# Optimization experiments

Measured on AMD Instinct MI355X. Metric: run time of the kernel, lower is better.

Reference implementation:

```python
import jax, jax.numpy as jnp
import numpy as np

SCALE = 8      # scale_factor from map_to_mat_info
PATCH = 32     # up_delta - low_delta + 1 == right_delta - left_delta + 1 (uniform interior patches)


def setup_inputs() -> dict:
    key = jax.random.key(0)
    mat_h, mat_w = 160, 160
    H = (mat_h - 1) * SCALE + PATCH  # 1304: deltas (0,31,0,31) -> no border clipping
    W = (mat_w - 1) * SCALE + PATCH
    x = jax.random.normal(key, (1, 3, H, W), dtype=jnp.float32)
    rgb_weight = jnp.array([0.299, 0.587, 0.114], dtype=jnp.float32).reshape(1, 3, 1, 1)
    return {"x": x, "rgb_weight": rgb_weight, "mat_h": mat_h, "mat_w": mat_w}


def reference(x, rgb_weight, mat_h, mat_w):
    P = PATCH
    # RGB -> grayscale (convert_gray branch for in_channels == 3)
    gray = jnp.sum(x * rgb_weight, axis=1)[0]  # (H, W)
    # Gather all overlapping PxP patches at stride SCALE -> (mat_h, mat_w, P, P)
    rows = (jnp.arange(mat_h) * SCALE)[:, None] + jnp.arange(P)[None, :]  # (mat_h, P)
    cols = (jnp.arange(mat_w) * SCALE)[:, None] + jnp.arange(P)[None, :]  # (mat_w, P)
    p = gray[rows.reshape(-1)].reshape(mat_h, P, -1)              # (mat_h, P, W)
    p = p[:, :, cols.reshape(-1)].reshape(mat_h, P, mat_w, P)     # (mat_h, P, mat_w, P)
    patches = jnp.transpose(p, (0, 2, 1, 3))                      # (mat_h, mat_w, P, P)
    # torch.rfft(signal_ndim=2, onesided=False) == full 2D FFT; power = re^2 + im^2
    F = jnp.fft.fft2(patches)
    log_power = jnp.log(F.real * F.real + F.imag * F.imag + 1.0)
    # High-frequency region sums (h == w == P, static)
    lo = P // 2 - P // 4 - 1   # 7
    up = P // 2 + P // 4       # 24
    r1 = jnp.sum(log_power[..., lo:up + 1, :], axis=(-2, -1))
    r2 = jnp.sum(log_power[..., up + 1:, lo:up + 1], axis=(-2, -1))
    r3 = jnp.sum(log_power[..., :lo, lo:up + 1], axis=(-2, -1))
    mat = (r1 + r2 + r3)[None, None]  # (1, 1, mat_h, mat_w)
    return mat / jnp.max(mat)
```

## Files before the change

### kernel.cpp

```cpp
#include <hip/hip_runtime.h>
#include <math.h>

#define SCALE 8
#define PSZ 32

__device__ constexpr float C32[16] = {
     1.000000000000000f,  0.980785280403230f,  0.923879532511287f,  0.831469612302545f,
     0.707106781186548f,  0.555570233019602f,  0.382683432365090f,  0.195090322016128f,
     0.000000000000000f, -0.195090322016128f, -0.382683432365090f, -0.555570233019602f,
    -0.707106781186548f, -0.831469612302545f, -0.923879532511287f, -0.980785280403230f };
__device__ constexpr float S32[16] = {
     0.000000000000000f,  0.195090322016128f,  0.382683432365090f,  0.555570233019602f,
     0.707106781186548f,  0.831469612302545f,  0.923879532511287f,  0.980785280403230f,
     1.000000000000000f,  0.980785280403230f,  0.923879532511287f,  0.831469612302545f,
     0.707106781186548f,  0.555570233019602f,  0.382683432365090f,  0.195090322016128f };

__device__ __forceinline__ constexpr int brev5(int i) {
    return ((i & 1) << 4) | ((i & 2) << 2) | (i & 4) | ((i & 8) >> 2) | ((i & 16) >> 4);
}

__device__ __forceinline__ void fft32(float re[PSZ], float im[PSZ]) {
#pragma unroll
    for (int i = 0; i < 32; ++i) {
        const int j = brev5(i);
        if (j > i) {
            float t = re[i]; re[i] = re[j]; re[j] = t;
            t = im[i]; im[i] = im[j]; im[j] = t;
        }
    }
#pragma unroll
    for (int s = 1; s <= 5; ++s) {
        const int m = 1 << s;
        const int h = m >> 1;
        const int tstep = 32 >> s;
#pragma unroll
        for (int k = 0; k < 32; k += m) {
#pragma unroll
            for (int j = 0; j < h; ++j) {
                const float wr = C32[j * tstep];
                const float wi = -S32[j * tstep];
                const int a = k + j;
                const int b = k + j + h;
                const float tr = wr * re[b] - wi * im[b];
                const float ti = wr * im[b] + wi * re[b];
                re[b] = re[a] - tr; im[b] = im[a] - ti;
                re[a] = re[a] + tr; im[a] = im[a] + ti;
            }
        }
    }
}

__device__ __forceinline__ unsigned pack_bf2(float hi, float lo) {
    const unsigned uh = __float_as_uint(hi) + 0x8000u;
    const unsigned ul = __float_as_uint(lo) + 0x8000u;
    return (uh & 0xFFFF0000u) | (ul >> 16);
}
__device__ __forceinline__ float bf_hi(unsigned u) { return __uint_as_float(u & 0xFFFF0000u); }
__device__ __forceinline__ float bf_lo(unsigned u) { return __uint_as_float(u << 16); }

__global__ __launch_bounds__(256) void gray_kernel(
        const float* __restrict__ x, const float* __restrict__ w,
        float* __restrict__ g, int n4, long long HW) {
    const int i = blockIdx.x * 256 + threadIdx.x;
    if (i >= n4) return;
    const float w0 = w[0], w1 = w[1], w2 = w[2];
    const float4 a = reinterpret_cast<const float4*>(x)[i];
    const float4 b = reinterpret_cast<const float4*>(x + HW)[i];
    const float4 c = reinterpret_cast<const float4*>(x + 2 * HW)[i];
    float4 o;
    o.x = w0 * a.x + w1 * b.x + w2 * c.x;
    o.y = w0 * a.y + w1 * b.y + w2 * c.y;
    o.z = w0 * a.z + w1 * b.z + w2 * c.z;
    o.w = w0 * a.w + w1 * b.w + w2 * c.w;
    reinterpret_cast<float4*>(g)[i] = o;
}

template <bool GRAY_PRE>
__global__ __launch_bounds__(128) void hfdft_patch_kernel(
        const float* __restrict__ x, const float* __restrict__ w,
        float* __restrict__ out, int H, int W, int mat_h, int mat_w) {
    __shared__ unsigned cb[8 * 528];

    const int tid = threadIdx.x;
    const int wid = tid >> 6;
    const int lane = tid & 63;
    const int P0 = blockIdx.x * 8 + wid * 4;
    const int total = mat_h * mat_w;
    const long long HW = (long long)H * W;
    unsigned* cbw = cb + wid * 4 * 528;

    {
        const int g = lane >> 5, r = lane & 31;
        int pA = P0 + 2 * g;
        if (pA > total - 1) pA = total - 1;
        int pB = pA + 1; if (pB > total - 1) pB = total - 1;
        const int phA = pA / mat_w, pwA = pA % mat_w;
        const int phB = pB / mat_w, pwB = pB % mat_w;
        const bool adj = (phA == phB) && (pwB == pwA + 1);

        float re[PSZ], im[PSZ];
        if (GRAY_PRE) {
            if (adj) {
                const int base = (phA * SCALE + r) * W + pwA * SCALE;
                const float4* g4 = reinterpret_cast<const float4*>(x + base);
                float win[40];
#pragma unroll
                for (int q = 0; q < 10; ++q) {
                    const float4 v = g4[q];
                    win[4 * q + 0] = v.x; win[4 * q + 1] = v.y;
                    win[4 * q + 2] = v.z; win[4 * q + 3] = v.w;
                }
#pragma unroll
                for (int i = 0; i < PSZ; ++i) { re[i] = win[i]; im[i] = win[i + 8]; }
            } else {
                const int baseA = (phA * SCALE + r) * W + pwA * SCALE;
                const int baseB = (phB * SCALE + r) * W + pwB * SCALE;
#pragma unroll
                for (int i = 0; i < PSZ; ++i) { re[i] = x[baseA + i]; im[i] = x[baseB + i]; }
            }
        } else {
            const float w0 = w[0], w1 = w[1], w2 = w[2];
            if (adj && ((W & 3) == 0)) {
                const int base = (phA * SCALE + r) * W + pwA * SCALE;
                const float4* a4 = reinterpret_cast<const float4*>(x + base);
                const float4* b4 = reinterpret_cast<const float4*>(x + HW + base);
                const float4* c4 = reinterpret_cast<const float4*>(x + 2 * HW + base);
                float win[40];
#pragma unroll
                for (int q = 0; q < 10; ++q) {
                    const float4 a = a4[q], b = b4[q], c = c4[q];
                    win[4 * q + 0] = w0 * a.x + w1 * b.x + w2 * c.x;
                    win[4 * q + 1] = w0 * a.y + w1 * b.y + w2 * c.y;
                    win[4 * q + 2] = w0 * a.z + w1 * b.z + w2 * c.z;
                    win[4 * q + 3] = w0 * a.w + w1 * b.w + w2 * c.w;
                }
#pragma unroll
                for (int i = 0; i < PSZ; ++i) { re[i] = win[i]; im[i] = win[i + 8]; }
            } else {
                const int baseA = (phA * SCALE + r) * W + pwA * SCALE;
                const int baseB = (phB * SCALE + r) * W + pwB * SCALE;
#pragma unroll
                for (int i = 0; i < PSZ; ++i) {
                    re[i] = w0 * x[baseA + i] + w1 * x[HW + baseA + i] + w2 * x[2 * HW + baseA + i];
                    im[i] = w0 * x[baseB + i] + w1 * x[HW + baseB + i] + w2 * x[2 * HW + baseB + i];
                }
            }
        }

        fft32(re, im);

        unsigned* cbA = cbw + (2 * g) * 528;
        unsigned* cbB = cbA + 528;
        cbA[r] = pack_bf2(re[0], re[16]);
        cbB[r] = pack_bf2(im[0], im[16]);
#pragma unroll
        for (int k = 1; k <= 15; ++k) {
            const int m = 32 - k;
            const float far_ = 0.5f * (re[k] + re[m]);
            const float fai_ = 0.5f * (im[k] - im[m]);
            const float fbr_ = 0.5f * (im[k] + im[m]);
            const float fbi_ = 0.5f * (re[m] - re[k]);
            cbA[k * 33 + r] = pack_bf2(far_, fai_);
            cbB[k * 33 + r] = pack_bf2(fbr_, fbi_);
        }
    }

    asm volatile("s_waitcnt lgkmcnt(0)" ::: "memory");

    {
        const int pl = lane >> 4, slot = lane & 15;
        const int p = P0 + pl;
        const unsigned* cbp = cbw + pl * 528 + slot * 33;

        float cre[PSZ], cim[PSZ];
#pragma unroll
        for (int r2 = 0; r2 < PSZ; ++r2) {
            const unsigned u = cbp[r2];
            cre[r2] = bf_hi(u);
            cim[r2] = bf_lo(u);
        }

        fft32(cre, cim);

        float s0 = 0.0f, s1 = 0.0f;
        if (slot == 0) {
#pragma unroll
            for (int kr = 0; kr <= 16; ++kr) {
                const int m = (32 - kr) & 31;
                const float g0r = 0.5f * (cre[kr] + cre[m]);
                const float g0i = 0.5f * (cim[kr] - cim[m]);
                const float g1r = 0.5f * (cim[kr] + cim[m]);
                const float g1i = 0.5f * (cre[m] - cre[kr]);
                const float w0c = (kr >= 7 ? 1.0f : 0.0f) + ((kr >= 8 && kr <= 15) ? 1.0f : 0.0f);
                const float w16c = 1.0f + ((kr >= 1 && kr <= 15) ? 1.0f : 0.0f);
                if (w0c > 0.0f)
                    s0 = fmaf(w0c, __logf(g0r * g0r + g0i * g0i + 1.0f), s0);
                s1 = fmaf(w16c, __logf(g1r * g1r + g1i * g1i + 1.0f), s1);
            }
        } else {
            const float b1f = (slot >= 7) ? 1.0f : 0.0f;
            const float m1f = (slot >= 8) ? 1.0f : 0.0f;
#pragma unroll
            for (int kr = 0; kr < 32; ++kr) {
                const float lp = __logf(cre[kr] * cre[kr] + cim[kr] * cim[kr] + 1.0f);
                float wgt;
                if (kr >= 8 && kr <= 24)      wgt = 2.0f;
                else if (kr == 7)             wgt = 1.0f + m1f;
                else if (kr == 25)            wgt = b1f + 1.0f;
                else                          wgt = b1f + m1f;
                if (kr & 1) s1 = fmaf(wgt, lp, s1);
                else        s0 = fmaf(wgt, lp, s0);
            }
        }
        float s = s0 + s1;

#pragma unroll
        for (int off = 8; off >= 1; off >>= 1) s += __shfl_xor(s, off, 16);
        if (slot == 0 && p < total) out[p] = s;
    }
}

__global__ __launch_bounds__(1024) void max_kernel(
        const float* __restrict__ sums, int n, unsigned* __restrict__ mx) {
    __shared__ float sm[16];
    float m = 0.0f;
    for (int i = blockIdx.x * 1024 + threadIdx.x; i < n; i += gridDim.x * 1024)
        m = fmaxf(m, sums[i]);
#pragma unroll
    for (int off = 32; off >= 1; off >>= 1) m = fmaxf(m, __shfl_xor(m, off, 64));
    if ((threadIdx.x & 63) == 0) sm[threadIdx.x >> 6] = m;
    __syncthreads();
    if (threadIdx.x == 0) {
#pragma unroll
        for (int i = 1; i < 16; ++i) m = fmaxf(m, sm[i]);
        atomicMax(mx, __float_as_uint(m));
    }
}

__global__ __launch_bounds__(256) void norm_kernel(
        float* __restrict__ out, int n, const unsigned* __restrict__ mx) {
    const int i = blockIdx.x * 256 + threadIdx.x;
    if (i < n) out[i] = out[i] / __uint_as_float(mx[0]);
}

extern "C" void kernel_launch(void* const* d_in, const int* in_sizes, int n_in,
                              void* d_out, int out_size, void* d_ws, size_t ws_size,
                              hipStream_t stream) {
    const float* x = (const float*)d_in[0];
    const float* w = (const float*)d_in[1];
    float* out = (float*)d_out;

    const int HWi = in_sizes[0] / 3;
    const int H = (int)(sqrt((double)HWi) + 0.5);
    const int W = H;
    const long long HW = (long long)H * W;
    const int mat = (int)(sqrt((double)out_size) + 0.5);
    const int total = mat * mat;
    const int blocksA = (total + 7) / 8;

    unsigned* maxbuf = (unsigned*)d_ws;
    float* gray = (float*)((char*)d_ws + 256);
    const size_t need = 256 + (size_t)HW * 4;

    hipMemsetAsync(maxbuf, 0, 4, stream);

    if (ws_size >= need && (W & 3) == 0) {
        const int n4 = (int)(HW / 4);
        hipLaunchKernelGGL(gray_kernel, dim3((n4 + 255) / 256), dim3(256), 0, stream,
                           x, w, gray, n4, HW);
        hipLaunchKernelGGL((hfdft_patch_kernel<true>), dim3(blocksA), dim3(128), 0, stream,
                           gray, w, out, H, W, mat, mat);
    } else {
        hipLaunchKernelGGL((hfdft_patch_kernel<false>), dim3(blocksA), dim3(128), 0, stream,
                           x, w, out, H, W, mat, mat);
    }
    hipLaunchKernelGGL(max_kernel, dim3(8), dim3(1024), 0, stream, out, total, maxbuf);
    hipLaunchKernelGGL(norm_kernel, dim3((total + 255) / 256), dim3(256), 0, stream,
                       out, total, maxbuf);
}
```

Baseline: 47.57 us.

## Split patch FFT into shared row-FFT pass and per-patch column-FFT pass

```diff
diff --git a/kernel.cpp b/kernel.cpp
--- a/kernel.cpp
+++ b/kernel.cpp
@@ -75,6 +75,112 @@
     reinterpret_cast<float4*>(g)[i] = o;
 }
 
+__global__ __launch_bounds__(256, 4) void rowfft_kernel(
+        const float* __restrict__ g, unsigned* __restrict__ spec,
+        int H, int W, int mat_w) {
+    const int cpairs = mat_w >> 1;
+    const int t = blockIdx.x * 256 + threadIdx.x;
+    if (t >= H * cpairs) return;
+    const int y = t / cpairs, cp = t - y * cpairs;
+    const int c0 = 2 * cp;
+
+    const float4* g4 = reinterpret_cast<const float4*>(g + (size_t)y * W + (size_t)c0 * SCALE);
+    float win[40];
+#pragma unroll
+    for (int q = 0; q < 10; ++q) {
+        const float4 v = g4[q];
+        win[4 * q + 0] = v.x; win[4 * q + 1] = v.y;
+        win[4 * q + 2] = v.z; win[4 * q + 3] = v.w;
+    }
+    float re[PSZ], im[PSZ];
+#pragma unroll
+    for (int i = 0; i < PSZ; ++i) { re[i] = win[i]; im[i] = win[i + 8]; }
+
+    fft32(re, im);
+
+    unsigned outA[16], outB[16];
+    outA[0] = pack_bf2(re[0], re[16]);
+    outB[0] = pack_bf2(im[0], im[16]);
+#pragma unroll
+    for (int k = 1; k <= 15; ++k) {
+        const int m = 32 - k;
+        const float far_ = 0.5f * (re[k] + re[m]);
+        const float fai_ = 0.5f * (im[k] - im[m]);
+        const float fbr_ = 0.5f * (im[k] + im[m]);
+        const float fbi_ = 0.5f * (re[m] - re[k]);
+        outA[k] = pack_bf2(far_, fai_);
+        outB[k] = pack_bf2(fbr_, fbi_);
+    }
+    uint4* s4 = reinterpret_cast<uint4*>(spec + ((size_t)y * mat_w + c0) * 16);
+#pragma unroll
+    for (int q = 0; q < 4; ++q)
+        s4[q] = make_uint4(outA[4 * q], outA[4 * q + 1], outA[4 * q + 2], outA[4 * q + 3]);
+#pragma unroll
+    for (int q = 0; q < 4; ++q)
+        s4[4 + q] = make_uint4(outB[4 * q], outB[4 * q + 1], outB[4 * q + 2], outB[4 * q + 3]);
+}
+
+__global__ __launch_bounds__(128, 4) void colfft_kernel(
+        const unsigned* __restrict__ spec, float* __restrict__ out,
+        int mat_h, int mat_w) {
+    const int tid = threadIdx.x;
+    const int wid = tid >> 6, lane = tid & 63;
+    const int pl = lane >> 4, slot = lane & 15;
+    const int total = mat_h * mat_w;
+    int p = blockIdx.x * 8 + wid * 4 + pl;
+    if (p > total - 1) p = total - 1;
+    const int ph = p / mat_w, pw = p - ph * mat_w;
+
+    const unsigned* sp = spec + ((size_t)(ph * SCALE) * mat_w + pw) * 16 + slot;
+    const size_t rstride = (size_t)mat_w * 16;
+
+    float cre[PSZ], cim[PSZ];
+#pragma unroll
+    for (int r2 = 0; r2 < PSZ; ++r2) {
+        const unsigned u = sp[r2 * rstride];
+        cre[r2] = bf_hi(u);
+        cim[r2] = bf_lo(u);
+    }
+
+    fft32(cre, cim);
+
+    float s0 = 0.0f, s1 = 0.0f;
+    if (slot == 0) {
+#pragma unroll
+        for (int kr = 0; kr <= 16; ++kr) {
+            const int m = (32 - kr) & 31;
+            const float g0r = 0.5f * (cre[kr] + cre[m]);
+            const float g0i = 0.5f * (cim[kr] - cim[m]);
+            const float g1r = 0.5f * (cim[kr] + cim[m]);
+            const float g1i = 0.5f * (cre[m] - cre[kr]);
+            const float w0c = (kr >= 7 ? 1.0f : 0.0f) + ((kr >= 8 && kr <= 15) ? 1.0f : 0.0f);
+            const float w16c = 1.0f + ((kr >= 1 && kr <= 15) ? 1.0f : 0.0f);
+            if (w0c > 0.0f)
+                s0 = fmaf(w0c, __logf(g0r * g0r + g0i * g0i + 1.0f), s0);
+            s1 = fmaf(w16c, __logf(g1r * g1r + g1i * g1i + 1.0f), s1);
+        }
+    } else {
+        const float b1f = (slot >= 7) ? 1.0f : 0.0f;
+        const float m1f = (slot >= 8) ? 1.0f : 0.0f;
+#pragma unroll
+        for (int kr = 0; kr < 32; ++kr) {
+            const float lp = __logf(cre[kr] * cre[kr] + cim[kr] * cim[kr] + 1.0f);
+            float wgt;
+            if (kr >= 8 && kr <= 24)      wgt = 2.0f;
+            else if (kr == 7)             wgt = 1.0f + m1f;
+            else if (kr == 25)            wgt = b1f + 1.0f;
+            else                          wgt = b1f + m1f;
+            if (kr & 1) s1 = fmaf(wgt, lp, s1);
+            else        s0 = fmaf(wgt, lp, s0);
+        }
+    }
+    float s = s0 + s1;
+
+#pragma unroll
+    for (int off = 8; off >= 1; off >>= 1) s += __shfl_xor(s, off, 16);
+    if (slot == 0) out[p] = s;
+}
+
 template <bool GRAY_PRE>
 __global__ __launch_bounds__(128) void hfdft_patch_kernel(
         const float* __restrict__ x, const float* __restrict__ w,
@@ -120,30 +226,12 @@
             }
         } else {
             const float w0 = w[0], w1 = w[1], w2 = w[2];
-            if (adj && ((W & 3) == 0)) {
-                const int base = (phA * SCALE + r) * W + pwA * SCALE;
-                const float4* a4 = reinterpret_cast<const float4*>(x + base);
-                const float4* b4 = reinterpret_cast<const float4*>(x + HW + base);
-                const float4* c4 = reinterpret_cast<const float4*>(x + 2 * HW + base);
-                float win[40];
-#pragma unroll
-                for (int q = 0; q < 10; ++q) {
-                    const float4 a = a4[q], b = b4[q], c = c4[q];
-                    win[4 * q + 0] = w0 * a.x + w1 * b.x + w2 * c.x;
-                    win[4 * q + 1] = w0 * a.y + w1 * b.y + w2 * c.y;
-                    win[4 * q + 2] = w0 * a.z + w1 * b.z + w2 * c.z;
-                    win[4 * q + 3] = w0 * a.w + w1 * b.w + w2 * c.w;
-                }
-#pragma unroll
-                for (int i = 0; i < PSZ; ++i) { re[i] = win[i]; im[i] = win[i + 8]; }
-            } else {
-                const int baseA = (phA * SCALE + r) * W + pwA * SCALE;
-                const int baseB = (phB * SCALE + r) * W + pwB * SCALE;
-#pragma unroll
-                for (int i = 0; i < PSZ; ++i) {
-                    re[i] = w0 * x[baseA + i] + w1 * x[HW + baseA + i] + w2 * x[2 * HW + baseA + i];
-                    im[i] = w0 * x[baseB + i] + w1 * x[HW + baseB + i] + w2 * x[2 * HW + baseB + i];
-                }
+            const int baseA = (phA * SCALE + r) * W + pwA * SCALE;
+            const int baseB = (phB * SCALE + r) * W + pwB * SCALE;
+#pragma unroll
+            for (int i = 0; i < PSZ; ++i) {
+                re[i] = w0 * x[baseA + i] + w1 * x[HW + baseA + i] + w2 * x[2 * HW + baseA + i];
+                im[i] = w0 * x[baseB + i] + w1 * x[HW + baseB + i] + w2 * x[2 * HW + baseB + i];
             }
         }
 
@@ -256,22 +344,35 @@
     const long long HW = (long long)H * W;
     const int mat = (int)(sqrt((double)out_size) + 0.5);
     const int total = mat * mat;
-    const int blocksA = (total + 7) / 8;
 
     unsigned* maxbuf = (unsigned*)d_ws;
     float* gray = (float*)((char*)d_ws + 256);
-    const size_t need = 256 + (size_t)HW * 4;
+    const size_t gray_bytes = (size_t)HW * 4;
+    unsigned* spec = (unsigned*)((char*)d_ws + 256 + gray_bytes);
+    const size_t spec_bytes = (size_t)H * mat * 16 * 4;
 
     hipMemsetAsync(maxbuf, 0, 4, stream);
 
-    if (ws_size >= need && (W & 3) == 0) {
+    const bool shape_ok = ((mat & 1) == 0) && (W == (mat - 1) * SCALE + PSZ)
+                          && (H == (mat - 1) * SCALE + PSZ) && ((W & 3) == 0);
+
+    if (shape_ok && ws_size >= 256 + gray_bytes + spec_bytes) {
         const int n4 = (int)(HW / 4);
         hipLaunchKernelGGL(gray_kernel, dim3((n4 + 255) / 256), dim3(256), 0, stream,
                            x, w, gray, n4, HW);
-        hipLaunchKernelGGL((hfdft_patch_kernel<true>), dim3(blocksA), dim3(128), 0, stream,
+        const int rowtasks = H * (mat >> 1);
+        hipLaunchKernelGGL(rowfft_kernel, dim3((rowtasks + 255) / 256), dim3(256), 0, stream,
+                           gray, spec, H, W, mat);
+        hipLaunchKernelGGL(colfft_kernel, dim3((total + 7) / 8), dim3(128), 0, stream,
+                           spec, out, mat, mat);
+    } else if (ws_size >= 256 + gray_bytes && (W & 3) == 0) {
+        const int n4 = (int)(HW / 4);
+        hipLaunchKernelGGL(gray_kernel, dim3((n4 + 255) / 256), dim3(256), 0, stream,
+                           x, w, gray, n4, HW);
+        hipLaunchKernelGGL((hfdft_patch_kernel<true>), dim3((total + 7) / 8), dim3(128), 0, stream,
                            gray, w, out, H, W, mat, mat);
     } else {
-        hipLaunchKernelGGL((hfdft_patch_kernel<false>), dim3(blocksA), dim3(128), 0, stream,
+        hipLaunchKernelGGL((hfdft_patch_kernel<false>), dim3((total + 7) / 8), dim3(128), 0, stream,
                            x, w, out, H, W, mat, mat);
     }
     hipLaunchKernelGGL(max_kernel, dim3(8), dim3(1024), 0, stream, out, total, maxbuf);
```

Measured after the change: 58.35 us. 22.6% more time.
